# Performance work log

Measured on AMD Instinct MI355X. Metric: run time of the kernel, lower is better.

The kernel has to match this reference:

```python
import jax, jax.numpy as jnp
import numpy as np

BETA = 0.25  # commitment_beta


def setup_inputs() -> dict:
    key = jax.random.key(0)
    k1, k2 = jax.random.split(key)
    B, C, H, W = 8, 256, 32, 32
    n_embed = 16384
    x = jax.random.normal(k1, (B, C, H, W), dtype=jnp.float32)
    # torch init: uniform_(-1/codebook_size, 1/codebook_size)
    weight = jax.random.uniform(k2, (n_embed, C), dtype=jnp.float32,
                                minval=-1.0 / n_embed, maxval=1.0 / n_embed)
    return {"x": x, "weight": weight}


def reference(x, weight):
    B, C, H, W = x.shape
    # b c h w -> b (h w) c
    xf = jnp.transpose(x, (0, 2, 3, 1)).reshape(B, H * W, C)
    flat = xf.reshape(-1, C)  # [N, C], N = B*H*W
    d = (jnp.sum(flat * flat, axis=1, keepdims=True)
         + jnp.sum(weight * weight, axis=1)[None, :]
         - 2.0 * flat @ weight.T)
    idx = jnp.argmin(d, axis=-1)          # [N]
    xq = weight[idx].reshape(B, H * W, C)  # codebook gather
    sg = jax.lax.stop_gradient
    loss = (BETA * jnp.mean((sg(xq) - xf) ** 2)
            + jnp.mean((xq - sg(xf)) ** 2))
    # straight-through estimator
    xq_st = xf + sg(xq - xf)
    # b (h w) c -> b c h w
    xq_img = jnp.transpose(xq_st.reshape(B, H, W, C), (0, 3, 1, 2))
    x_code = idx.reshape(B, H, W)
    return xq_img, loss, x_code
```

## Files before the change

kernel.cpp:

```cpp
#include <hip/hip_runtime.h>
#include <stdint.h>

#define NROW    8192
#define CDIM    256
#define NCODE   16384
#define MARGINF 6.0e-5f

typedef short short8 __attribute__((ext_vector_type(8)));
typedef float floatx4 __attribute__((ext_vector_type(4)));

__device__ inline ushort f2bf(float f) {
    unsigned u = __builtin_bit_cast(unsigned, f);
    unsigned r = (u + 0x7fffu + ((u >> 16) & 1u)) >> 16;
    return (ushort)r;
}
__device__ inline unsigned fsort(float v) {
    unsigned u = __builtin_bit_cast(unsigned, v);
    return (u >> 31) ? ~u : (u | 0x80000000u);
}

__device__ inline void gl_lds16(const ushort* g, ushort* lds) {
    __builtin_amdgcn_global_load_lds(
        (const __attribute__((address_space(1))) unsigned int*)(g),
        (__attribute__((address_space(3))) unsigned int*)(lds),
        16, 0, 0);
}

__global__ __launch_bounds__(256) void prep_all(const float* __restrict__ x,
                                                const float* __restrict__ w,
                                                float* __restrict__ xf32,
                                                ushort* __restrict__ xbf,
                                                ushort* __restrict__ wbf,
                                                float* __restrict__ S2a) {
#pragma clang fp contract(off)
    const int bid = blockIdx.x;
    const int t = threadIdx.x;
    if (bid < 2048) {
        __shared__ float tile[32][33];
        const int b = bid & 7, ht = (bid >> 3) & 31, ct = bid >> 8;
        const int hw0 = ht * 32, c0 = ct * 32;
        {
            const int cc = t >> 5, hh = t & 31;
            #pragma unroll
            for (int i = 0; i < 4; ++i) {
                int cl = cc + i * 8;
                tile[cl][hh] = x[((size_t)(b * 256 + c0 + cl) << 10) + hw0 + hh];
            }
        }
        __syncthreads();
        {
            const int col = t & 31, row = t >> 5;
            #pragma unroll
            for (int i = 0; i < 4; ++i) {
                int r = row + i * 8;
                float v = tile[col][r];
                size_t o = ((size_t)(b * 1024 + hw0 + r) << 8) + c0 + col;
                xf32[o] = v;
                xbf[o] = f2bf(v);
            }
        }
    } else {
        const int gt = (bid - 2048) * 256 + t;
        const int j = gt >> 4, l16 = gt & 15;
        const int h = l16 >> 3, ai = l16 & 7;
        const float* a = w + ((size_t)j << 8);
        float v = a[h * 128 + ai];
        float racc = v * v;
        for (int i = 8; i < 128; i += 8) {
            v = a[h * 128 + ai + i];
            racc = racc + v * v;
        }
        racc = racc + __shfl_xor(racc, 1);
        racc = racc + __shfl_xor(racc, 2);
        racc = racc + __shfl_xor(racc, 4);
        racc = racc + __shfl_xor(racc, 8);
        if (l16 == 0) S2a[j] = racc;
        const float* seg = a + l16 * 16;
        ushort* oseg = wbf + ((size_t)j << 8) + l16 * 16;
        #pragma unroll
        for (int i = 0; i < 16; i += 8) {
            ushort u8[8];
            #pragma unroll
            for (int k = 0; k < 8; ++k) u8[k] = f2bf(seg[i + k]);
            *(ushort4*)(oseg + i)     = make_ushort4(u8[0], u8[1], u8[2], u8[3]);
            *(ushort4*)(oseg + i + 4) = make_ushort4(u8[4], u8[5], u8[6], u8[7]);
        }
    }
}

__global__ __launch_bounds__(256) void gemm_min(const ushort* __restrict__ Wb,
                                                const ushort* __restrict__ Xb,
                                                const float* __restrict__ S2a,
                                                unsigned* __restrict__ bm32) {
    __shared__ __attribute__((aligned(16))) ushort As[8192];
    __shared__ __attribute__((aligned(16))) ushort Bs[8192];
    __shared__ __attribute__((aligned(16))) unsigned stg32[128][2];

    const int n0 = blockIdx.x * 128;
    const int j0 = blockIdx.y * 128;
    const int t  = threadIdx.x;
    const int wv = t >> 6, l = t & 63;
    const int wr = wv >> 1, wc = wv & 1;
    const int q  = l >> 4, c = l & 15;

    const int lr = l >> 3;
    const int lperm = (l & 7) ^ lr;
    const size_t gA0 = ((size_t)(j0 + wv * 32 + lr) << 8) + lperm * 8;
    const size_t gB0 = ((size_t)(n0 + wv * 32 + lr) << 8) + lperm * 8;
    const int ldsbase = wv * 2048;

    floatx4 acc[4][4];
    #pragma unroll
    for (int mi = 0; mi < 4; ++mi)
        #pragma unroll
        for (int ni = 0; ni < 4; ++ni)
            acc[mi][ni] = (floatx4){0.f, 0.f, 0.f, 0.f};

    for (int kb = 0; kb < 4; ++kb) {
        if (kb) __syncthreads();
        #pragma unroll
        for (int ca = 0; ca < 4; ++ca) {
            gl_lds16(Wb + gA0 + ca * 2048 + kb * 64, As + ldsbase + ca * 512);
            gl_lds16(Xb + gB0 + ca * 2048 + kb * 64, Bs + ldsbase + ca * 512);
        }
        __syncthreads();
        #pragma unroll
        for (int kk = 0; kk < 2; ++kk) {
            short8 af[4], bf[4];
            #pragma unroll
            for (int mi = 0; mi < 4; ++mi) {
                int row = wr * 64 + mi * 16 + c;
                int pos = (kk * 4 + q) ^ (c & 7);
                af[mi] = *(const short8*)&As[row * 64 + pos * 8];
            }
            #pragma unroll
            for (int ni = 0; ni < 4; ++ni) {
                int row = wc * 64 + ni * 16 + c;
                int pos = (kk * 4 + q) ^ (c & 7);
                bf[ni] = *(const short8*)&Bs[row * 64 + pos * 8];
            }
            #pragma unroll
            for (int mi = 0; mi < 4; ++mi)
                #pragma unroll
                for (int ni = 0; ni < 4; ++ni)
                    acc[mi][ni] = __builtin_amdgcn_mfma_f32_16x16x32_bf16(
                        af[mi], bf[ni], acc[mi][ni], 0, 0, 0);
        }
    }

    float4 s2v[4];
    #pragma unroll
    for (int mi = 0; mi < 4; ++mi)
        s2v[mi] = *(const float4*)&S2a[j0 + wr * 64 + mi * 16 + (q << 2)];

    #pragma unroll
    for (int ni = 0; ni < 4; ++ni) {
        float M1 = 0.f, M2 = 0.f; int I1 = 0;
        #pragma unroll
        for (int mi = 0; mi < 4; ++mi) {
            float v0 = fmaf(-2.f, acc[mi][ni][0], s2v[mi].x);
            float v1 = fmaf(-2.f, acc[mi][ni][1], s2v[mi].y);
            float v2 = fmaf(-2.f, acc[mi][ni][2], s2v[mi].z);
            float v3 = fmaf(-2.f, acc[mi][ni][3], s2v[mi].w);
            float lo01 = fminf(v0, v1), hi01 = fmaxf(v0, v1);
            float lo23 = fminf(v2, v3), hi23 = fmaxf(v2, v3);
            int i01 = v1 < v0 ? 1 : 0;
            int i23 = v3 < v2 ? 3 : 2;
            float m1 = fminf(lo01, lo23);
            float m2 = fminf(fmaxf(lo01, lo23), lo23 < lo01 ? hi23 : hi01);
            int idx = mi * 16 + (q << 2) + (lo23 < lo01 ? i23 : i01);
            if (mi == 0) { M1 = m1; M2 = m2; I1 = idx; }
            else {
                float nM2 = (m1 < M1) ? fminf(M1, m2) : fminf(M2, m1);
                I1 = (m1 < M1) ? idx : I1;
                M1 = fminf(M1, m1);
                M2 = nM2;
            }
        }
        #pragma unroll
        for (int off = 16; off <= 32; off <<= 1) {
            float oM1 = __shfl_xor(M1, off);
            float oM2 = __shfl_xor(M2, off);
            int   oI1 = __shfl_xor(I1, off);
            float nM2 = fminf(fminf(M2, oM2), fmaxf(M1, oM1));
            bool take = (oM1 < M1) || (oM1 == M1 && oI1 < I1);
            I1 = take ? oI1 : I1;
            M1 = fminf(M1, oM1);
            M2 = nM2;
        }
        if (q == 0) {
            ushort min16 = __builtin_bit_cast(ushort, (_Float16)M1);
            float delta = M2 - M1;
            ushort d16 = __builtin_bit_cast(ushort, (_Float16)delta);
            ushort d8 = d16 >> 8;
            float rec = (float)__builtin_bit_cast(_Float16, (ushort)(d8 << 8));
            if (rec > delta && d8) d8--;
            stg32[wc * 64 + ni * 16 + c][wr] =
                ((unsigned)min16 << 16) | ((unsigned)d8 << 8) | (unsigned)I1;
        }
    }
    __syncthreads();
    if (t < 128) {
        uint2 v = *(const uint2*)&stg32[t][0];
        *(uint2*)(bm32 + ((size_t)(n0 + t) << 8) + blockIdx.y * 2) = v;
    }
}

__global__ __launch_bounds__(256) void rescore8(const unsigned* __restrict__ bm32,
                                                const float* __restrict__ xf32,
                                                const float* __restrict__ w,
                                                const float* __restrict__ S2a,
                                                int* __restrict__ idxb,
                                                float* __restrict__ xcode,
                                                float* __restrict__ lpart) {
#pragma clang fp contract(off)
    __shared__ float xs[4][256];
    __shared__ short sing[4][128];
    __shared__ short blk[4][16];
    __shared__ int ns[4], nb[4];

    const int t = threadIdx.x, wv = t >> 6, l = t & 63;
    const int n = blockIdx.x * 4 + wv;
    if (l == 0) { ns[wv] = 0; nb[wv] = 0; }

    const float4 xv = *(const float4*)&xf32[((size_t)n << 8) + l * 4];
    *(float4*)&xs[wv][l * 4] = xv;

    const uint4 e = *(const uint4*)(bm32 + ((size_t)n << 8) + l * 4);
    unsigned ee[4] = {e.x, e.y, e.z, e.w};
    float vals[4];
    #pragma unroll
    for (int i = 0; i < 4; ++i)
        vals[i] = (float)__builtin_bit_cast(_Float16, (ushort)(ee[i] >> 16));
    float vmin = fminf(fminf(vals[0], vals[1]), fminf(vals[2], vals[3]));
    #pragma unroll
    for (int off = 1; off <= 32; off <<= 1) vmin = fminf(vmin, __shfl_xor(vmin, off));
    const float thr = vmin + MARGINF;
    #pragma unroll
    for (int i = 0; i < 4; ++i) {
        if (vals[i] <= thr) {
            const int jb = l * 4 + i;
            int p = atomicAdd(&ns[wv], 1);
            if (p < 128) sing[wv][p] = (short)(jb * 64 + (int)(ee[i] & 63u));
            float dr = (float)__builtin_bit_cast(_Float16,
                           (ushort)(((ee[i] >> 8) & 0xFFu) << 8));
            if (vals[i] + dr <= thr) {
                int pb = atomicAdd(&nb[wv], 1);
                if (pb < 16) blk[wv][pb] = (short)jb;
            }
        }
    }

    float racc = 0.f;
    if (l < 16) {
        const float* a_ = &xs[wv][(l >> 3) * 128];
        const int ai = l & 7;
        float v = a_[ai];
        racc = v * v;
        for (int i = 8; i < 128; i += 8) { v = a_[i + ai]; racc = racc + v * v; }
    }
    racc = racc + __shfl_xor(racc, 1);
    racc = racc + __shfl_xor(racc, 2);
    racc = racc + __shfl_xor(racc, 4);
    racc = racc + __shfl_xor(racc, 8);
    const float S1n = __shfl(racc, 0);

    const int nsv = ns[wv] < 128 ? ns[wv] : 128;
    const int nbv = nb[wv] < 16 ? nb[wv] : 16;
    const int ntot = nsv + nbv * 64;
    unsigned long long best = ~0ull;
    for (int s = l; s < ntot; s += 64) {
        const int j = (s < nsv)
            ? (int)sing[wv][s]
            : (int)blk[wv][(s - nsv) >> 6] * 64 + ((s - nsv) & 63);
        const float4* wr4 = (const float4*)(w + ((size_t)j << 8));
        float g = 0.f;
        #pragma unroll
        for (int half = 0; half < 4; ++half) {
            float4 buf[16];
            #pragma unroll
            for (int i = 0; i < 16; ++i) buf[i] = wr4[half * 16 + i];
            #pragma unroll
            for (int i = 0; i < 16; ++i) {
                const float4 xv4 = *(const float4*)&xs[wv][half * 64 + i * 4];
                g = fmaf(xv4.x, buf[i].x, g);
                g = fmaf(xv4.y, buf[i].y, g);
                g = fmaf(xv4.z, buf[i].z, g);
                g = fmaf(xv4.w, buf[i].w, g);
            }
        }
        float d = (S1n + S2a[j]) - 2.0f * g;
        unsigned long long key = ((unsigned long long)fsort(d) << 32) | (unsigned)j;
        if (key < best) best = key;
    }
    #pragma unroll
    for (int off = 1; off <= 32; off <<= 1) {
        unsigned long long o = __shfl_xor(best, off);
        if (o < best) best = o;
    }
    const int J = (int)(best & 0xffffffffu);

    const float4 wj = *(const float4*)&w[((size_t)J << 8) + l * 4];
    float d0 = wj.x - xv.x, d1 = wj.y - xv.y, d2 = wj.z - xv.z, d3 = wj.w - xv.w;
    float lacc = (d0 * d0 + d1 * d1) + (d2 * d2 + d3 * d3);
    #pragma unroll
    for (int off = 1; off <= 32; off <<= 1) lacc += __shfl_xor(lacc, off);
    if (l == 0) {
        idxb[n] = J;
        xcode[n] = (float)J;
        lpart[n] = lacc;
    }
}

__global__ __launch_bounds__(256) void outputs_k(const float* __restrict__ w,
                                                 const int* __restrict__ idxb,
                                                 const float* __restrict__ lpart,
                                                 float* __restrict__ out,
                                                 float* __restrict__ loss) {
    __shared__ float tile[32][33];
    __shared__ int ids[32];
    const int b = blockIdx.x, ht = blockIdx.y, ct = blockIdx.z;
    const int t = threadIdx.x;
    const int hw0 = ht * 32, c0 = ct * 32;
    if (t < 32) ids[t] = idxb[(b << 10) + hw0 + t];
    __syncthreads();
    {
        const int nl = t & 31, cq = t >> 5;
        float4 v = *(const float4*)&w[((size_t)ids[nl] << 8) + c0 + cq * 4];
        tile[nl][cq * 4]     = v.x;
        tile[nl][cq * 4 + 1] = v.y;
        tile[nl][cq * 4 + 2] = v.z;
        tile[nl][cq * 4 + 3] = v.w;
    }
    __syncthreads();
    {
        const int hwl = t & 31, cq = t >> 5;
        #pragma unroll
        for (int i = 0; i < 4; ++i) {
            const int cl = cq * 4 + i;
            out[((size_t)((b << 8) + c0 + cl) << 10) + hw0 + hwl] = tile[hwl][cl];
        }
    }
    if (b == 0 && ht == 0 && ct == 0) {
        __shared__ float red[256];
        float s = 0.f;
        for (int i = 0; i < 32; ++i) s += lpart[t + (i << 8)];
        red[t] = s;
        __syncthreads();
        for (int k = 128; k > 0; k >>= 1) {
            if (t < k) red[t] += red[t + k];
            __syncthreads();
        }
        if (t == 0) *loss = red[0] * (1.25f / 2097152.0f);
    }
}

extern "C" void kernel_launch(void* const* d_in, const int* in_sizes, int n_in,
                              void* d_out, int out_size, void* d_ws, size_t ws_size,
                              hipStream_t stream) {
    const float* x = (const float*)d_in[0];
    const float* w = (const float*)d_in[1];
    float* out = (float*)d_out;

    char* ws = (char*)d_ws;
    const size_t MB = 1024u * 1024u;
    ushort*   xbf   = (ushort*)  (ws);
    float*    xf32  = (float*)   (ws + 4 * MB);
    ushort*   wbf   = (ushort*)  (ws + 12 * MB);
    float*    S2a   = (float*)   (ws + 20 * MB);
    unsigned* bm32  = (unsigned*)(ws + 21 * MB);
    int*      idxb  = (int*)     (ws + 29 * MB);
    float*    lpart = (float*)   (ws + 29 * MB + 65536);

    float* loss_ptr  = out + 2097152;
    float* xcode_ptr = out + 2097153;

    prep_all<<<dim3(3072),      256, 0, stream>>>(x, w, xf32, xbf, wbf, S2a);
    gemm_min<<<dim3(64, 128),   256, 0, stream>>>(wbf, xbf, S2a, bm32);
    rescore8<<<dim3(2048),      256, 0, stream>>>(bm32, xf32, w, S2a, idxb,
                                                  xcode_ptr, lpart);
    outputs_k<<<dim3(8, 32, 8), 256, 0, stream>>>(w, idxb, lpart, out, loss_ptr);
}
```

Baseline: 248.6 us.

## Fuse rescore with output gather, transpose and loss reduction via last-block counter

Merges the rescore and output kernels: each block now handles 16 rows, keeps the chosen codebook rows in LDS, writes the transposed output tile directly, and reduces the loss through an atomic counter whose last block does the final sum. This removes a kernel launch and the idx round-trip through global memory. The prep kernel also switches the codebook bf16 conversion to float4 loads. In exchange the rescore grid shrinks from 2048 to 512 blocks with each wave processing 4 rows serially, which lowers parallelism in the candidate-rescoring phase.

```diff
diff --git a/kernel.cpp b/kernel.cpp
--- a/kernel.cpp
+++ b/kernel.cpp
@@ -31,7 +31,8 @@
                                                 float* __restrict__ xf32,
                                                 ushort* __restrict__ xbf,
                                                 ushort* __restrict__ wbf,
-                                                float* __restrict__ S2a) {
+                                                float* __restrict__ S2a,
+                                                int* __restrict__ ctr) {
 #pragma clang fp contract(off)
     const int bid = blockIdx.x;
     const int t = threadIdx.x;
@@ -60,6 +61,7 @@
             }
         }
     } else {
+        if (bid == 2048 && t == 0) *ctr = 0;
         const int gt = (bid - 2048) * 256 + t;
         const int j = gt >> 4, l16 = gt & 15;
         const int h = l16 >> 3, ai = l16 & 7;
@@ -75,15 +77,13 @@
         racc = racc + __shfl_xor(racc, 4);
         racc = racc + __shfl_xor(racc, 8);
         if (l16 == 0) S2a[j] = racc;
-        const float* seg = a + l16 * 16;
+        const float4* seg4 = (const float4*)(a + l16 * 16);
         ushort* oseg = wbf + ((size_t)j << 8) + l16 * 16;
         #pragma unroll
-        for (int i = 0; i < 16; i += 8) {
-            ushort u8[8];
-            #pragma unroll
-            for (int k = 0; k < 8; ++k) u8[k] = f2bf(seg[i + k]);
-            *(ushort4*)(oseg + i)     = make_ushort4(u8[0], u8[1], u8[2], u8[3]);
-            *(ushort4*)(oseg + i + 4) = make_ushort4(u8[4], u8[5], u8[6], u8[7]);
+        for (int i = 0; i < 4; ++i) {
+            float4 vv = seg4[i];
+            *(ushort4*)(oseg + i * 4) =
+                make_ushort4(f2bf(vv.x), f2bf(vv.y), f2bf(vv.z), f2bf(vv.w));
         }
     }
 }
@@ -206,145 +206,151 @@
     }
 }
 
-__global__ __launch_bounds__(256) void rescore8(const unsigned* __restrict__ bm32,
+__global__ __launch_bounds__(256) void rescore9(const unsigned* __restrict__ bm32,
                                                 const float* __restrict__ xf32,
                                                 const float* __restrict__ w,
                                                 const float* __restrict__ S2a,
-                                                int* __restrict__ idxb,
+                                                float* __restrict__ out,
                                                 float* __restrict__ xcode,
-                                                float* __restrict__ lpart) {
+                                                float* __restrict__ lpart,
+                                                int* __restrict__ ctr,
+                                                float* __restrict__ loss) {
 #pragma clang fp contract(off)
-    __shared__ float xs[4][256];
+    __shared__ float xs[16][256];
+    __shared__ float wt[16][260];
     __shared__ short sing[4][128];
     __shared__ short blk[4][16];
     __shared__ int ns[4], nb[4];
+    __shared__ float lred[4];
+    __shared__ int lastf;
+    __shared__ float red[256];
 
     const int t = threadIdx.x, wv = t >> 6, l = t & 63;
-    const int n = blockIdx.x * 4 + wv;
-    if (l == 0) { ns[wv] = 0; nb[wv] = 0; }
-
-    const float4 xv = *(const float4*)&xf32[((size_t)n << 8) + l * 4];
-    *(float4*)&xs[wv][l * 4] = xv;
-
-    const uint4 e = *(const uint4*)(bm32 + ((size_t)n << 8) + l * 4);
-    unsigned ee[4] = {e.x, e.y, e.z, e.w};
-    float vals[4];
-    #pragma unroll
-    for (int i = 0; i < 4; ++i)
-        vals[i] = (float)__builtin_bit_cast(_Float16, (ushort)(ee[i] >> 16));
-    float vmin = fminf(fminf(vals[0], vals[1]), fminf(vals[2], vals[3]));
-    #pragma unroll
-    for (int off = 1; off <= 32; off <<= 1) vmin = fminf(vmin, __shfl_xor(vmin, off));
-    const float thr = vmin + MARGINF;
+    const int n0 = blockIdx.x * 16;
+
     #pragma unroll
     for (int i = 0; i < 4; ++i) {
-        if (vals[i] <= thr) {
-            const int jb = l * 4 + i;
-            int p = atomicAdd(&ns[wv], 1);
-            if (p < 128) sing[wv][p] = (short)(jb * 64 + (int)(ee[i] & 63u));
-            float dr = (float)__builtin_bit_cast(_Float16,
-                           (ushort)(((ee[i] >> 8) & 0xFFu) << 8));
-            if (vals[i] + dr <= thr) {
-                int pb = atomicAdd(&nb[wv], 1);
-                if (pb < 16) blk[wv][pb] = (short)jb;
-            }
-        }
-    }
-
-    float racc = 0.f;
-    if (l < 16) {
-        const float* a_ = &xs[wv][(l >> 3) * 128];
-        const int ai = l & 7;
-        float v = a_[ai];
-        racc = v * v;
-        for (int i = 8; i < 128; i += 8) { v = a_[i + ai]; racc = racc + v * v; }
-    }
-    racc = racc + __shfl_xor(racc, 1);
-    racc = racc + __shfl_xor(racc, 2);
-    racc = racc + __shfl_xor(racc, 4);
-    racc = racc + __shfl_xor(racc, 8);
-    const float S1n = __shfl(racc, 0);
-
-    const int nsv = ns[wv] < 128 ? ns[wv] : 128;
-    const int nbv = nb[wv] < 16 ? nb[wv] : 16;
-    const int ntot = nsv + nbv * 64;
-    unsigned long long best = ~0ull;
-    for (int s = l; s < ntot; s += 64) {
-        const int j = (s < nsv)
-            ? (int)sing[wv][s]
-            : (int)blk[wv][(s - nsv) >> 6] * 64 + ((s - nsv) & 63);
-        const float4* wr4 = (const float4*)(w + ((size_t)j << 8));
-        float g = 0.f;
-        #pragma unroll
-        for (int half = 0; half < 4; ++half) {
-            float4 buf[16];
-            #pragma unroll
-            for (int i = 0; i < 16; ++i) buf[i] = wr4[half * 16 + i];
-            #pragma unroll
-            for (int i = 0; i < 16; ++i) {
-                const float4 xv4 = *(const float4*)&xs[wv][half * 64 + i * 4];
-                g = fmaf(xv4.x, buf[i].x, g);
-                g = fmaf(xv4.y, buf[i].y, g);
-                g = fmaf(xv4.z, buf[i].z, g);
-                g = fmaf(xv4.w, buf[i].w, g);
-            }
-        }
-        float d = (S1n + S2a[j]) - 2.0f * g;
-        unsigned long long key = ((unsigned long long)fsort(d) << 32) | (unsigned)j;
-        if (key < best) best = key;
-    }
-    #pragma unroll
-    for (int off = 1; off <= 32; off <<= 1) {
-        unsigned long long o = __shfl_xor(best, off);
-        if (o < best) best = o;
-    }
-    const int J = (int)(best & 0xffffffffu);
-
-    const float4 wj = *(const float4*)&w[((size_t)J << 8) + l * 4];
-    float d0 = wj.x - xv.x, d1 = wj.y - xv.y, d2 = wj.z - xv.z, d3 = wj.w - xv.w;
-    float lacc = (d0 * d0 + d1 * d1) + (d2 * d2 + d3 * d3);
-    #pragma unroll
-    for (int off = 1; off <= 32; off <<= 1) lacc += __shfl_xor(lacc, off);
-    if (l == 0) {
-        idxb[n] = J;
-        xcode[n] = (float)J;
-        lpart[n] = lacc;
-    }
-}
-
-__global__ __launch_bounds__(256) void outputs_k(const float* __restrict__ w,
-                                                 const int* __restrict__ idxb,
-                                                 const float* __restrict__ lpart,
-                                                 float* __restrict__ out,
-                                                 float* __restrict__ loss) {
-    __shared__ float tile[32][33];
-    __shared__ int ids[32];
-    const int b = blockIdx.x, ht = blockIdx.y, ct = blockIdx.z;
-    const int t = threadIdx.x;
-    const int hw0 = ht * 32, c0 = ct * 32;
-    if (t < 32) ids[t] = idxb[(b << 10) + hw0 + t];
+        float4 v = *(const float4*)&xf32[((size_t)n0 << 8) + i * 1024 + t * 4];
+        *(float4*)&xs[0][i * 1024 + t * 4] = v;
+    }
     __syncthreads();
+
+    float wavloss = 0.f;
+    for (int rr = 0; rr < 4; ++rr) {
+        const int row = wv * 4 + rr;
+        const int n = n0 + row;
+        if (l == 0) { ns[wv] = 0; nb[wv] = 0; }
+
+        const uint4 e = *(const uint4*)(bm32 + ((size_t)n << 8) + l * 4);
+        unsigned ee[4] = {e.x, e.y, e.z, e.w};
+        float vals[4];
+        #pragma unroll
+        for (int i = 0; i < 4; ++i)
+            vals[i] = (float)__builtin_bit_cast(_Float16, (ushort)(ee[i] >> 16));
+        float vmin = fminf(fminf(vals[0], vals[1]), fminf(vals[2], vals[3]));
+        #pragma unroll
+        for (int off = 1; off <= 32; off <<= 1)
+            vmin = fminf(vmin, __shfl_xor(vmin, off));
+        const float thr = vmin + MARGINF;
+        #pragma unroll
+        for (int i = 0; i < 4; ++i) {
+            if (vals[i] <= thr) {
+                const int jb = l * 4 + i;
+                int p = atomicAdd(&ns[wv], 1);
+                if (p < 128) sing[wv][p] = (short)(jb * 64 + (int)(ee[i] & 63u));
+                float dr = (float)__builtin_bit_cast(_Float16,
+                               (ushort)(((ee[i] >> 8) & 0xFFu) << 8));
+                if (vals[i] + dr <= thr) {
+                    int pb = atomicAdd(&nb[wv], 1);
+                    if (pb < 16) blk[wv][pb] = (short)jb;
+                }
+            }
+        }
+
+        float racc = 0.f;
+        if (l < 16) {
+            const float* a_ = &xs[row][(l >> 3) * 128];
+            const int ai = l & 7;
+            float v = a_[ai];
+            racc = v * v;
+            for (int i = 8; i < 128; i += 8) { v = a_[i + ai]; racc = racc + v * v; }
+        }
+        racc = racc + __shfl_xor(racc, 1);
+        racc = racc + __shfl_xor(racc, 2);
+        racc = racc + __shfl_xor(racc, 4);
+        racc = racc + __shfl_xor(racc, 8);
+        const float S1n = __shfl(racc, 0);
+
+        const int nsv = ns[wv] < 128 ? ns[wv] : 128;
+        const int nbv = nb[wv] < 16 ? nb[wv] : 16;
+        const int ntot = nsv + nbv * 64;
+        unsigned long long best = ~0ull;
+        for (int s = l; s < ntot; s += 64) {
+            const int j = (s < nsv)
+                ? (int)sing[wv][s]
+                : (int)blk[wv][(s - nsv) >> 6] * 64 + ((s - nsv) & 63);
+            const float4* wr4 = (const float4*)(w + ((size_t)j << 8));
+            float g = 0.f;
+            #pragma unroll
+            for (int half = 0; half < 4; ++half) {
+                float4 buf[16];
+                #pragma unroll
+                for (int i = 0; i < 16; ++i) buf[i] = wr4[half * 16 + i];
+                #pragma unroll
+                for (int i = 0; i < 16; ++i) {
+                    const float4 xv4 = *(const float4*)&xs[row][half * 64 + i * 4];
+                    g = fmaf(xv4.x, buf[i].x, g);
+                    g = fmaf(xv4.y, buf[i].y, g);
+                    g = fmaf(xv4.z, buf[i].z, g);
+                    g = fmaf(xv4.w, buf[i].w, g);
+                }
+            }
+            float d = (S1n + S2a[j]) - 2.0f * g;
+            unsigned long long key = ((unsigned long long)fsort(d) << 32) | (unsigned)j;
+            if (key < best) best = key;
+        }
+        #pragma unroll
+        for (int off = 1; off <= 32; off <<= 1) {
+            unsigned long long o = __shfl_xor(best, off);
+            if (o < best) best = o;
+        }
+        const int J = (int)(best & 0xffffffffu);
+        if (l == 0) xcode[n] = (float)J;
+
+        const float4 wj = *(const float4*)&w[((size_t)J << 8) + l * 4];
+        *(float4*)&wt[row][l * 4] = wj;
+        const float4 xv4 = *(const float4*)&xs[row][l * 4];
+        float d0 = wj.x - xv4.x, d1 = wj.y - xv4.y;
+        float d2 = wj.z - xv4.z, d3 = wj.w - xv4.w;
+        wavloss += (d0 * d0 + d1 * d1) + (d2 * d2 + d3 * d3);
+    }
+    #pragma unroll
+    for (int off = 1; off <= 32; off <<= 1) wavloss += __shfl_xor(wavloss, off);
+    if (l == 0) lred[wv] = wavloss;
+    __syncthreads();
+
     {
-        const int nl = t & 31, cq = t >> 5;
-        float4 v = *(const float4*)&w[((size_t)ids[nl] << 8) + c0 + cq * 4];
-        tile[nl][cq * 4]     = v.x;
-        tile[nl][cq * 4 + 1] = v.y;
-        tile[nl][cq * 4 + 2] = v.z;
-        tile[nl][cq * 4 + 3] = v.w;
+        const int b = n0 >> 10, hw0 = n0 & 1023;
+        float* ob = out + (((size_t)((b << 8) + t)) << 10) + hw0;
+        float v[16];
+        #pragma unroll
+        for (int r = 0; r < 16; ++r) v[r] = wt[r][t];
+        *(float4*)(ob)      = make_float4(v[0],  v[1],  v[2],  v[3]);
+        *(float4*)(ob + 4)  = make_float4(v[4],  v[5],  v[6],  v[7]);
+        *(float4*)(ob + 8)  = make_float4(v[8],  v[9],  v[10], v[11]);
+        *(float4*)(ob + 12) = make_float4(v[12], v[13], v[14], v[15]);
+    }
+
+    if (t == 0) {
+        lpart[blockIdx.x] = (lred[0] + lred[1]) + (lred[2] + lred[3]);
+        __threadfence();
+        int old = atomicAdd(ctr, 1);
+        lastf = (old == 511) ? 1 : 0;
     }
     __syncthreads();
-    {
-        const int hwl = t & 31, cq = t >> 5;
-        #pragma unroll
-        for (int i = 0; i < 4; ++i) {
-            const int cl = cq * 4 + i;
-            out[((size_t)((b << 8) + c0 + cl) << 10) + hw0 + hwl] = tile[hwl][cl];
-        }
-    }
-    if (b == 0 && ht == 0 && ct == 0) {
-        __shared__ float red[256];
-        float s = 0.f;
-        for (int i = 0; i < 32; ++i) s += lpart[t + (i << 8)];
+    if (lastf) {
+        __threadfence();
+        float s = lpart[t] + lpart[t + 256];
         red[t] = s;
         __syncthreads();
         for (int k = 128; k > 0; k >>= 1) {
@@ -369,15 +375,14 @@
     ushort*   wbf   = (ushort*)  (ws + 12 * MB);
     float*    S2a   = (float*)   (ws + 20 * MB);
     unsigned* bm32  = (unsigned*)(ws + 21 * MB);
-    int*      idxb  = (int*)     (ws + 29 * MB);
-    float*    lpart = (float*)   (ws + 29 * MB + 65536);
+    float*    lpart = (float*)   (ws + 29 * MB);
+    int*      ctr   = (int*)     (ws + 29 * MB + 8192);
 
     float* loss_ptr  = out + 2097152;
     float* xcode_ptr = out + 2097153;
 
-    prep_all<<<dim3(3072),      256, 0, stream>>>(x, w, xf32, xbf, wbf, S2a);
-    gemm_min<<<dim3(64, 128),   256, 0, stream>>>(wbf, xbf, S2a, bm32);
-    rescore8<<<dim3(2048),      256, 0, stream>>>(bm32, xf32, w, S2a, idxb,
-                                                  xcode_ptr, lpart);
-    outputs_k<<<dim3(8, 32, 8), 256, 0, stream>>>(w, idxb, lpart, out, loss_ptr);
-}
+    prep_all<<<dim3(3072),     256, 0, stream>>>(x, w, xf32, xbf, wbf, S2a, ctr);
+    gemm_min<<<dim3(64, 128),  256, 0, stream>>>(wbf, xbf, S2a, bm32);
+    rescore9<<<dim3(512),      256, 0, stream>>>(bm32, xf32, w, S2a, out,
+                                                 xcode_ptr, lpart, ctr, loss_ptr);
+}
```

Result: slower. 264.7 us (+6.5%).
